# Kernel tuning notes

Hardware: AMD Instinct MI355X
Metric: run time of the kernel (lower is better)

## Reference

```python
import jax, jax.numpy as jnp
import numpy as np

B, S, D, H, E, K = 4, 512, 512, 2048, 8, 2
LN_EPS = 1e-5

def _ln(x, g, b):
    m = jnp.mean(x, axis=-1, keepdims=True)
    v = jnp.var(x, axis=-1, keepdims=True)
    return (x - m) / jnp.sqrt(v + LN_EPS) * g + b

def setup_inputs() -> dict:
    key = jax.random.key(0)
    ks = jax.random.split(key, 8)
    s = 0.02
    return {
        "x": jax.random.normal(ks[0], (B, S, D), dtype=jnp.float32),
        "context": jax.random.normal(ks[1], (B, S, D), dtype=jnp.float32),
        "quality": jax.random.uniform(ks[2], (B, 1), dtype=jnp.float32),
        "rn_g": jnp.ones((D,), jnp.float32), "rn_b": jnp.zeros((D,), jnp.float32),
        "cn_g": jnp.ones((D,), jnp.float32), "cn_b": jnp.zeros((D,), jnp.float32),
        "ctx_W": jax.random.normal(ks[3], (D, D), dtype=jnp.float32) * s,
        "ctx_b": jnp.zeros((D,), jnp.float32),
        "qual_W": jax.random.normal(ks[4], (1, D), dtype=jnp.float32) * s,
        "qual_b": jnp.zeros((D,), jnp.float32),
        "rtr_W": jax.random.normal(ks[5], (D, E), dtype=jnp.float32) * s,
        "rtr_b": jnp.zeros((E,), jnp.float32),
        "temperature": jnp.asarray(1.0, jnp.float32),
        "W1": jax.random.normal(ks[6], (E, D, H), dtype=jnp.float32) * s,
        "b1": jnp.zeros((E, H), jnp.float32),
        "W2": jax.random.normal(ks[7], (E, H, D), dtype=jnp.float32) * s,
        "b2": jnp.zeros((E, D), jnp.float32),
    }

def reference(x, context, quality, rn_g, rn_b, cn_g, cn_b, ctx_W, ctx_b,
              qual_W, qual_b, rtr_W, rtr_b, temperature, W1, b1, W2, b2):
    # router features: LN(x) + context_proj(LN(context)) + quality_proj(quality)
    rf = _ln(x, rn_g, rn_b) + (_ln(context, cn_g, cn_b) @ ctx_W + ctx_b)
    q = quality[:, None, :]                      # [B,1,1]
    rf = rf + (q @ qual_W + qual_b)              # broadcast [B,1,D] over seq
    logits = (rf @ rtr_W + rtr_b) / jnp.maximum(temperature, 0.25)  # [B,S,E]
    # eval mode: no router noise, no dropout
    topk_logits, topk_idx = jax.lax.top_k(logits, K)
    gates = jax.nn.softmax(topk_logits, axis=-1)                    # [B,S,K]
    # per-token per-expert combine weight (equivalent to masked dispatch)
    combine = jnp.sum(gates[..., None] * jax.nn.one_hot(topk_idx, E, dtype=x.dtype), axis=-2)  # [B,S,E]
    # dense all-expert FFN, combined with (mostly zero) gate weights
    h = jax.nn.gelu(jnp.einsum('bsd,edh->bseh', x, W1) + b1, approximate=False)  # [B,S,E,H]
    y = jnp.einsum('bseh,ehd->bsed', h, W2) + b2                                 # [B,S,E,D]
    out = jnp.einsum('bsed,bse->bsd', y, combine)
    # aux losses
    probs = jax.nn.softmax(logits, axis=-1)
    importance = probs.mean(axis=(0, 1))
    load_balance = jnp.mean((importance - 1.0 / E) ** 2)
    router_z = jnp.mean(jax.scipy.special.logsumexp(logits, axis=-1) ** 2)
    entropy = jnp.mean(-jnp.sum(probs * jnp.log(jnp.clip(probs, 1e-9, None)), axis=-1))
    aux = load_balance + 1e-3 * router_z - 1e-3 * entropy
    return out, load_balance, router_z, entropy, aux
```

## Files before the change

kernel.cpp:

```cpp
#include <hip/hip_runtime.h>
#include <hip/hip_bf16.h>
#include <math.h>

#define Bb 4
#define Ss 512
#define Dd 512
#define Hh 2048
#define Ee 8
#define TOKENS 2048
#define CAP 2048

typedef __attribute__((ext_vector_type(8))) _Float16 f16x8;
typedef __attribute__((ext_vector_type(4))) _Float16 f16x4;
typedef __attribute__((ext_vector_type(4))) float f32x4;

#define WS_CNT   0
#define WS_OFFS  32
#define WS_M1    128
#define WS_QV    16512
#define WS_CB    16544
#define WS_LIST  16640
#define WS_GLIST 82176
#define WS_LOG   147712
#define WS_XF    (WS_LOG + 65536)
#define WS_W1F   (WS_XF + 2097152)
#define WS_W2F   (WS_W1F + 16777216)
#define WS_HF    (WS_W2F + 16777216)
#define WS_YB    (WS_HF + 16777216)
#define WS_SEL   (WS_YB + 16777216)

__device__ __forceinline__ float wred(float v) {
#pragma unroll
  for (int o = 32; o > 0; o >>= 1) v += __shfl_down(v, o);
  return v;
}

__device__ __forceinline__ float wredx(float v) {
#pragma unroll
  for (int o = 32; o > 0; o >>= 1) v += __shfl_xor(v, o);
  return v;
}

__device__ __forceinline__ float block_sum(float v, float* s4, int tid) {
  v = wred(v);
  __syncthreads();
  if ((tid & 63) == 0) s4[tid >> 6] = v;
  __syncthreads();
  return s4[0] + s4[1] + s4[2] + s4[3];
}

__device__ __forceinline__ float gelu_f(float v) {
  return 0.5f * v * (1.0f + erff(v * 0.7071067811865475f));
}

#define GL16(gp, lp) __builtin_amdgcn_global_load_lds( \
    (const __attribute__((address_space(1))) void*)(gp), \
    (__attribute__((address_space(3))) void*)(lp), 16, 0, 0)

__device__ __forceinline__ void convT_tile(const float* __restrict__ src,
    _Float16* __restrict__ dst, int R, int C, int bx, float* ls) {
  int nr = R >> 6, ncc = C >> 6;
  int e = bx / (nr * ncc);
  int rem = bx % (nr * ncc);
  int rt = rem / ncc, ct = rem % ncc;
  int tid = threadIdx.x;
  const float* s0 = src + (size_t)e * R * C + (size_t)(rt * 64) * C + ct * 64;
#pragma unroll
  for (int j = 0; j < 4; j++) {
    int li = j * 256 + tid;
    int rr = li >> 4, c4 = (li & 15) << 2;
    float4 v = *(const float4*)(s0 + (size_t)rr * C + c4);
    ls[rr * 65 + c4] = v.x;
    ls[rr * 65 + c4 + 1] = v.y;
    ls[rr * 65 + c4 + 2] = v.z;
    ls[rr * 65 + c4 + 3] = v.w;
  }
  __syncthreads();
#pragma unroll
  for (int j = 0; j < 4; j++) {
    int li = j * 256 + tid;
    int on = li >> 4, k4 = (li & 15) << 2;
    f16x4 o;
    o[0] = (_Float16)ls[(k4 + 0) * 65 + on];
    o[1] = (_Float16)ls[(k4 + 1) * 65 + on];
    o[2] = (_Float16)ls[(k4 + 2) * 65 + on];
    o[3] = (_Float16)ls[(k4 + 3) * 65 + on];
    *(f16x4*)(dst + ((size_t)e * C + ct * 64 + on) * R + rt * 64 + k4) = o;
  }
}

__global__ __launch_bounds__(256) void k_pre(
    const float* __restrict__ ctx_W, const float* __restrict__ rtr_W,
    const float* __restrict__ rtr_b, const float* __restrict__ qual_W,
    const float* __restrict__ qual_b, const float* __restrict__ ctx_b,
    const float* __restrict__ W1, const float* __restrict__ W2,
    float* __restrict__ M1, float* __restrict__ qv, float* __restrict__ cb,
    _Float16* __restrict__ w1f, _Float16* __restrict__ w2f) {
  __shared__ float ls[64 * 65];
  int bx = blockIdx.x;
  if (bx >= 513) {
    int cx = bx - 513;
    if (cx < Ee * 8 * 32) convT_tile(W1, w1f, Dd, Hh, cx, ls);
    else convT_tile(W2, w2f, Hh, Dd, cx - Ee * 8 * 32, ls);
    return;
  }
  int d = bx;
  int tid = threadIdx.x;
  if (tid >= 64) return;
  int lane = tid;
  if (d < Dd) {
    float acc[Ee] = {0.f, 0.f, 0.f, 0.f, 0.f, 0.f, 0.f, 0.f};
    for (int k = lane; k < Dd; k += 64) {
      float cw = ctx_W[d * Dd + k];
      const float* r = rtr_W + k * Ee;
#pragma unroll
      for (int e = 0; e < Ee; e++) acc[e] += cw * r[e];
    }
#pragma unroll
    for (int e = 0; e < Ee; e++) acc[e] = wred(acc[e]);
    if (lane == 0) {
#pragma unroll
      for (int e = 0; e < Ee; e++) M1[d * Ee + e] = acc[e];
    }
  } else {
    float aq[Ee] = {0.f, 0.f, 0.f, 0.f, 0.f, 0.f, 0.f, 0.f};
    float ab[Ee] = {0.f, 0.f, 0.f, 0.f, 0.f, 0.f, 0.f, 0.f};
    for (int k = lane; k < Dd; k += 64) {
      float qw = qual_W[k];
      float bb = ctx_b[k] + qual_b[k];
      const float* r = rtr_W + k * Ee;
#pragma unroll
      for (int e = 0; e < Ee; e++) {
        aq[e] += qw * r[e];
        ab[e] += bb * r[e];
      }
    }
#pragma unroll
    for (int e = 0; e < Ee; e++) {
      aq[e] = wred(aq[e]);
      ab[e] = wred(ab[e]);
    }
    if (lane == 0) {
#pragma unroll
      for (int e = 0; e < Ee; e++) {
        qv[e] = aq[e];
        cb[e] = ab[e] + rtr_b[e];
      }
    }
  }
}

__global__ __launch_bounds__(256) void k_logits(
    const float* __restrict__ x, const float* __restrict__ ctx,
    const float* __restrict__ quality, const float* __restrict__ rn_g,
    const float* __restrict__ rn_b, const float* __restrict__ cn_g,
    const float* __restrict__ cn_b, const float* __restrict__ rtr_W,
    const float* __restrict__ M1, const float* __restrict__ qv,
    const float* __restrict__ cb, const float* __restrict__ temperature,
    float* __restrict__ logitsS, _Float16* __restrict__ xf) {
  int wid = threadIdx.x >> 6, lane = threadIdx.x & 63;
  int t = blockIdx.x * 4 + wid;
  int d0 = lane * 8;

  float xv[8], cv[8];
  *(float4*)&xv[0] = *(const float4*)(x + (size_t)t * Dd + d0);
  *(float4*)&xv[4] = *(const float4*)(x + (size_t)t * Dd + d0 + 4);
  *(float4*)&cv[0] = *(const float4*)(ctx + (size_t)t * Dd + d0);
  *(float4*)&cv[4] = *(const float4*)(ctx + (size_t)t * Dd + d0 + 4);

  f16x8 xh;
#pragma unroll
  for (int d = 0; d < 8; d++) xh[d] = (_Float16)xv[d];
  *(f16x8*)(xf + (size_t)t * Dd + d0) = xh;

  float sx = 0.f, sc = 0.f;
#pragma unroll
  for (int d = 0; d < 8; d++) { sx += xv[d]; sc += cv[d]; }
  float mx = wredx(sx) * (1.f / Dd);
  float mc = wredx(sc) * (1.f / Dd);
  float vx = 0.f, vc = 0.f;
#pragma unroll
  for (int d = 0; d < 8; d++) {
    vx += (xv[d] - mx) * (xv[d] - mx);
    vc += (cv[d] - mc) * (cv[d] - mc);
  }
  float rsx = rsqrtf(wredx(vx) * (1.f / Dd) + 1e-5f);
  float rsc = rsqrtf(wredx(vc) * (1.f / Dd) + 1e-5f);

  float rg[8], rb[8], cg[8], cbb[8];
  *(float4*)&rg[0] = *(const float4*)(rn_g + d0);
  *(float4*)&rg[4] = *(const float4*)(rn_g + d0 + 4);
  *(float4*)&rb[0] = *(const float4*)(rn_b + d0);
  *(float4*)&rb[4] = *(const float4*)(rn_b + d0 + 4);
  *(float4*)&cg[0] = *(const float4*)(cn_g + d0);
  *(float4*)&cg[4] = *(const float4*)(cn_g + d0 + 4);
  *(float4*)&cbb[0] = *(const float4*)(cn_b + d0);
  *(float4*)&cbb[4] = *(const float4*)(cn_b + d0 + 4);

  float lg[Ee] = {0.f, 0.f, 0.f, 0.f, 0.f, 0.f, 0.f, 0.f};
#pragma unroll
  for (int d = 0; d < 8; d++) {
    float xn = (xv[d] - mx) * rsx * rg[d] + rb[d];
    float cn = (cv[d] - mc) * rsc * cg[d] + cbb[d];
    float rw[8], m1[8];
    *(float4*)&rw[0] = *(const float4*)(rtr_W + (size_t)(d0 + d) * Ee);
    *(float4*)&rw[4] = *(const float4*)(rtr_W + (size_t)(d0 + d) * Ee + 4);
    *(float4*)&m1[0] = *(const float4*)(M1 + (size_t)(d0 + d) * Ee);
    *(float4*)&m1[4] = *(const float4*)(M1 + (size_t)(d0 + d) * Ee + 4);
#pragma unroll
    for (int e = 0; e < Ee; e++) lg[e] += xn * rw[e] + cn * m1[e];
  }
#pragma unroll
  for (int e = 0; e < Ee; e++) lg[e] = wredx(lg[e]);

  if (lane == 0) {
    float invT = 1.f / fmaxf(temperature[0], 0.25f);
    float q = quality[t / Ss];
    float L[8];
#pragma unroll
    for (int e = 0; e < Ee; e++) L[e] = (lg[e] + q * qv[e] + cb[e]) * invT;
    *(float4*)(logitsS + (size_t)t * Ee) = *(float4*)&L[0];
    *(float4*)(logitsS + (size_t)t * Ee + 4) = *(float4*)&L[4];
  }
}

__global__ __launch_bounds__(256) void k_select(
    const float* __restrict__ logitsS, int* __restrict__ cnt,
    int* __restrict__ offs, int* __restrict__ list,
    float* __restrict__ glist, int* __restrict__ sel,
    float* __restrict__ out) {
  __shared__ int scnt[Ee];
  __shared__ float s4[4];
  int tid = threadIdx.x;
  if (tid < Ee) scnt[tid] = 0;
  __syncthreads();

  float impL[Ee] = {0.f, 0.f, 0.f, 0.f, 0.f, 0.f, 0.f, 0.f};
  float zL = 0.f, eL = 0.f;

#pragma unroll
  for (int j = 0; j < 8; j++) {
    int t = j * 256 + tid;
    float L[8];
    *(float4*)&L[0] = *(const float4*)(logitsS + (size_t)t * Ee);
    *(float4*)&L[4] = *(const float4*)(logitsS + (size_t)t * Ee + 4);

    int i0 = 0;
#pragma unroll
    for (int e = 1; e < Ee; e++)
      if (L[e] > L[i0]) i0 = e;
    int i1 = (i0 == 0) ? 1 : 0;
#pragma unroll
    for (int e = 0; e < Ee; e++)
      if (e != i0 && L[e] > L[i1]) i1 = e;

    float e1 = __expf(L[i1] - L[i0]);
    float g0 = 1.f / (1.f + e1);
    float g1 = e1 / (1.f + e1);

    float m = L[i0];
    float p[8];
    float sum = 0.f;
#pragma unroll
    for (int e = 0; e < Ee; e++) {
      p[e] = __expf(L[e] - m);
      sum += p[e];
    }
    float lse = m + __logf(sum);
    float inv = 1.f / sum;
    zL += lse * lse;
#pragma unroll
    for (int e = 0; e < Ee; e++) {
      p[e] *= inv;
      eL -= p[e] * __logf(fmaxf(p[e], 1e-9f));
      impL[e] += p[e];
    }

    int s0 = atomicAdd(&scnt[i0], 1);
    list[i0 * CAP + s0] = t;
    glist[i0 * CAP + s0] = g0;
    sel[t * 2 + 0] = (i0 << 12) | s0;
    int s1 = atomicAdd(&scnt[i1], 1);
    list[i1 * CAP + s1] = t;
    glist[i1 * CAP + s1] = g1;
    sel[t * 2 + 1] = (i1 << 12) | s1;
  }

  float impS[Ee];
#pragma unroll
  for (int e = 0; e < Ee; e++) impS[e] = block_sum(impL[e], s4, tid);
  float zS = block_sum(zL, s4, tid);
  float eS = block_sum(eL, s4, tid);
  __syncthreads();

  if (tid == 0) {
    int s = 0;
#pragma unroll
    for (int e = 0; e < Ee; e++) {
      cnt[e] = scnt[e];
      offs[e] = s;
      s += scnt[e];
    }
    float lb = 0.f;
#pragma unroll
    for (int e = 0; e < Ee; e++) {
      float v = impS[e] * (1.f / TOKENS) - (1.f / Ee);
      lb += v * v;
    }
    lb *= (1.f / Ee);
    float rz = zS * (1.f / TOKENS);
    float en = eS * (1.f / TOKENS);
    float* sp = out + (size_t)Bb * Ss * Dd;
    sp[0] = lb;
    sp[1] = rz;
    sp[2] = en;
    sp[3] = lb + 0.001f * rz - 0.001f * en;
  }
}

__global__ __launch_bounds__(256) void k_mg1(
    const _Float16* __restrict__ xf, const _Float16* __restrict__ w1f,
    const float* __restrict__ b1,
    const int* __restrict__ cnt, const int* __restrict__ offs,
    const int* __restrict__ list, _Float16* __restrict__ hf) {
  int bx = blockIdx.x;
  int e = bx >> 8;
  int r = (bx >> 4) & 15;
  int c = bx & 15;
  int ne = cnt[e];
  if (r * 128 >= ne) return;
  int off = offs[e];

  __shared__ _Float16 As[8 * 128 * 8];
  __shared__ _Float16 Bs[8 * 128 * 8];
  __shared__ int stok[128];

  int tid = threadIdx.x;
  if (tid < 128) {
    int row = r * 128 + tid;
    stok[tid] = list[e * CAP + ((row < ne) ? row : (ne - 1))];
  }
  __syncthreads();

  size_t asrc[4], bsrc[4];
  int lq[4];
#pragma unroll
  for (int q = 0; q < 4; q++) {
    int idx = q * 256 + tid;
    int g = idx >> 7, row = idx & 127;
    asrc[q] = (size_t)stok[row] * Dd + g * 8;
    bsrc[q] = ((size_t)(e * Hh + c * 128 + row)) * Dd + g * 8;
    lq[q] = idx * 8;
  }

  int lane = tid & 63, wid = tid >> 6;
  int wm = wid >> 1, wn = wid & 1;
  int l15 = lane & 15, lg = lane >> 4;

  f32x4 acc[4][4] = {};

  for (int k0 = 0; k0 < Dd; k0 += 64) {
#pragma unroll
    for (int q = 0; q < 4; q++) {
      GL16(xf + asrc[q] + k0, &As[lq[q]]);
      GL16(w1f + bsrc[q] + k0, &Bs[lq[q]]);
    }
    __syncthreads();
    f16x8 a[2][4], b[2][4];
#pragma unroll
    for (int ks = 0; ks < 2; ks++) {
#pragma unroll
      for (int m = 0; m < 4; m++)
        a[ks][m] = *(const f16x8*)&As[(((ks * 4 + lg) << 7) + wm * 64 + m * 16 + l15) * 8];
#pragma unroll
      for (int n = 0; n < 4; n++)
        b[ks][n] = *(const f16x8*)&Bs[(((ks * 4 + lg) << 7) + wn * 64 + n * 16 + l15) * 8];
    }
#pragma unroll
    for (int ks = 0; ks < 2; ks++)
#pragma unroll
      for (int m = 0; m < 4; m++)
#pragma unroll
        for (int n = 0; n < 4; n++)
          acc[m][n] = __builtin_amdgcn_mfma_f32_16x16x32_f16(a[ks][m], b[ks][n], acc[m][n], 0, 0, 0);
    __syncthreads();
  }

  int lg4 = lg * 4;
#pragma unroll
  for (int n = 0; n < 4; n++) {
    int colg = c * 128 + wn * 64 + n * 16 + l15;
    float bias = b1[e * Hh + colg];
#pragma unroll
    for (int m = 0; m < 4; m++) {
#pragma unroll
      for (int j = 0; j < 4; j++) {
        int rowl = r * 128 + wm * 64 + m * 16 + lg4 + j;
        if (rowl < ne)
          hf[(size_t)(off + rowl) * Hh + colg] = (_Float16)gelu_f(acc[m][n][j] + bias);
      }
    }
  }
}

__global__ __launch_bounds__(256) void k_mg2(
    const _Float16* __restrict__ hf, const _Float16* __restrict__ w2f,
    const int* __restrict__ cnt, const int* __restrict__ offs,
    _Float16* __restrict__ yb) {
  int bx = blockIdx.x;
  int e = bx >> 8;
  int r = (bx >> 4) & 15;
  int c = (bx >> 2) & 3;
  int kS = bx & 3;
  int ne = cnt[e];
  if (r * 128 >= ne) return;
  int off = offs[e];

  __shared__ _Float16 As[8 * 128 * 8];
  __shared__ _Float16 Bs[8 * 128 * 8];

  int tid = threadIdx.x;
  size_t kbase = (size_t)kS * 512;

  size_t asrc[4], bsrc[4];
  int lq[4];
#pragma unroll
  for (int q = 0; q < 4; q++) {
    int idx = q * 256 + tid;
    int g = idx >> 7, row = idx & 127;
    int ar = r * 128 + row;
    if (ar >= ne) ar = ne - 1;
    asrc[q] = (size_t)(off + ar) * Hh + kbase + g * 8;
    bsrc[q] = ((size_t)(e * Dd + c * 128 + row)) * Hh + kbase + g * 8;
    lq[q] = idx * 8;
  }

  int lane = tid & 63, wid = tid >> 6;
  int wm = wid >> 1, wn = wid & 1;
  int l15 = lane & 15, lg = lane >> 4;

  f32x4 acc[4][4] = {};

  for (int k0 = 0; k0 < 512; k0 += 64) {
#pragma unroll
    for (int q = 0; q < 4; q++) {
      GL16(hf + asrc[q] + k0, &As[lq[q]]);
      GL16(w2f + bsrc[q] + k0, &Bs[lq[q]]);
    }
    __syncthreads();
    f16x8 a[2][4], b[2][4];
#pragma unroll
    for (int ks = 0; ks < 2; ks++) {
#pragma unroll
      for (int m = 0; m < 4; m++)
        a[ks][m] = *(const f16x8*)&As[(((ks * 4 + lg) << 7) + wm * 64 + m * 16 + l15) * 8];
#pragma unroll
      for (int n = 0; n < 4; n++)
        b[ks][n] = *(const f16x8*)&Bs[(((ks * 4 + lg) << 7) + wn * 64 + n * 16 + l15) * 8];
    }
#pragma unroll
    for (int ks = 0; ks < 2; ks++)
#pragma unroll
      for (int m = 0; m < 4; m++)
#pragma unroll
        for (int n = 0; n < 4; n++)
          acc[m][n] = __builtin_amdgcn_mfma_f32_16x16x32_f16(a[ks][m], b[ks][n], acc[m][n], 0, 0, 0);
    __syncthreads();
  }

  int lg4 = lg * 4;
#pragma unroll
  for (int m = 0; m < 4; m++) {
#pragma unroll
    for (int j = 0; j < 4; j++) {
      int rowl = r * 128 + wm * 64 + m * 16 + lg4 + j;
      if (rowl < ne) {
        _Float16* yp = yb + ((size_t)kS * 4096 + off + rowl) * Dd;
#pragma unroll
        for (int n = 0; n < 4; n++) {
          int colg = c * 128 + wn * 64 + n * 16 + l15;
          yp[colg] = (_Float16)acc[m][n][j];
        }
      }
    }
  }
}

__global__ __launch_bounds__(256) void k_comb(
    const _Float16* __restrict__ yb, const int* __restrict__ sel,
    const float* __restrict__ glist, const int* __restrict__ offs,
    const float* __restrict__ b2, float* __restrict__ out) {
  int t = blockIdx.x * 4 + (threadIdx.x >> 6);
  int lane = threadIdx.x & 63;
  int c0 = lane * 8;

  float acc[8] = {0.f, 0.f, 0.f, 0.f, 0.f, 0.f, 0.f, 0.f};
#pragma unroll
  for (int k = 0; k < 2; k++) {
    int pk = sel[t * 2 + k];
    int e = pk >> 12, pos = pk & 4095;
    int slot = offs[e] + pos;
    float g = glist[e * CAP + pos];
    float pa[8] = {0.f, 0.f, 0.f, 0.f, 0.f, 0.f, 0.f, 0.f};
#pragma unroll
    for (int s = 0; s < 4; s++) {
      f16x8 v = *(const f16x8*)(yb + ((size_t)s * 4096 + slot) * Dd + c0);
#pragma unroll
      for (int j = 0; j < 8; j++) pa[j] += (float)v[j];
    }
    const float* bb = b2 + e * Dd + c0;
    float b4[8];
    *(float4*)&b4[0] = *(const float4*)bb;
    *(float4*)&b4[4] = *(const float4*)(bb + 4);
#pragma unroll
    for (int j = 0; j < 8; j++) acc[j] += g * (pa[j] + b4[j]);
  }
  float* op = out + (size_t)t * Dd + c0;
  *(float4*)op = *(float4*)&acc[0];
  *(float4*)(op + 4) = *(float4*)&acc[4];
}

extern "C" void kernel_launch(void* const* d_in, const int* in_sizes, int n_in,
                              void* d_out, int out_size, void* d_ws, size_t ws_size,
                              hipStream_t stream) {
  const float* x = (const float*)d_in[0];
  const float* ctx = (const float*)d_in[1];
  const float* quality = (const float*)d_in[2];
  const float* rn_g = (const float*)d_in[3];
  const float* rn_b = (const float*)d_in[4];
  const float* cn_g = (const float*)d_in[5];
  const float* cn_b = (const float*)d_in[6];
  const float* ctx_W = (const float*)d_in[7];
  const float* ctx_b = (const float*)d_in[8];
  const float* qual_W = (const float*)d_in[9];
  const float* qual_b = (const float*)d_in[10];
  const float* rtr_W = (const float*)d_in[11];
  const float* rtr_b = (const float*)d_in[12];
  const float* temperature = (const float*)d_in[13];
  const float* W1 = (const float*)d_in[14];
  const float* b1 = (const float*)d_in[15];
  const float* W2 = (const float*)d_in[16];
  const float* b2 = (const float*)d_in[17];
  float* out = (float*)d_out;

  char* w = (char*)d_ws;
  int* cnt = (int*)(w + WS_CNT);
  int* offs = (int*)(w + WS_OFFS);
  float* M1 = (float*)(w + WS_M1);
  float* qv = (float*)(w + WS_QV);
  float* cb = (float*)(w + WS_CB);
  int* list = (int*)(w + WS_LIST);
  float* glist = (float*)(w + WS_GLIST);
  float* logitsS = (float*)(w + WS_LOG);
  _Float16* xf = (_Float16*)(w + WS_XF);
  _Float16* w1f = (_Float16*)(w + WS_W1F);
  _Float16* w2f = (_Float16*)(w + WS_W2F);
  _Float16* hf = (_Float16*)(w + WS_HF);
  _Float16* yb = (_Float16*)(w + WS_YB);
  int* sel = (int*)(w + WS_SEL);

  k_pre<<<513 + Ee * 8 * 32 * 2, 256, 0, stream>>>(
      ctx_W, rtr_W, rtr_b, qual_W, qual_b, ctx_b, W1, W2, M1, qv, cb, w1f, w2f);
  k_logits<<<TOKENS / 4, 256, 0, stream>>>(x, ctx, quality, rn_g, rn_b, cn_g, cn_b, rtr_W,
                                           M1, qv, cb, temperature, logitsS, xf);
  k_select<<<1, 256, 0, stream>>>(logitsS, cnt, offs, list, glist, sel, out);
  k_mg1<<<Ee * 16 * 16, 256, 0, stream>>>(xf, w1f, b1, cnt, offs, list, hf);
  k_mg2<<<Ee * 16 * 4 * 4, 256, 0, stream>>>(hf, w2f, cnt, offs, yb);
  k_comb<<<TOKENS / 4, 256, 0, stream>>>(yb, sel, glist, offs, b2, out);
}
```

Before: 256.7 us.

## Pad expert segments to tiles, pre-gather tokens, and move routing math into logits kernel

The top-k selection, gates and aux-loss statistics are now computed per token in the logits kernel, with per-block partial sums, so the single-block select kernel only does the scatter and a small reduction. Each expert segment is padded to a multiple of 128 rows, and a new gather kernel copies the routed token rows contiguously. The GEMM kernels therefore use a compact grid over padded tiles with contiguous A loads and no row bounds checks. In exchange there is an extra gather pass plus wasted work on padding rows, but far fewer empty blocks are launched and the serial single-block work shrinks.

```diff
diff --git a/kernel.cpp b/kernel.cpp
--- a/kernel.cpp
+++ b/kernel.cpp
@@ -9,25 +9,29 @@
 #define Ee 8
 #define TOKENS 2048
 #define CAP 2048
+#define SLOTS 5120
 
 typedef __attribute__((ext_vector_type(8))) _Float16 f16x8;
 typedef __attribute__((ext_vector_type(4))) _Float16 f16x4;
 typedef __attribute__((ext_vector_type(4))) float f32x4;
 
 #define WS_CNT   0
-#define WS_OFFS  32
-#define WS_M1    128
-#define WS_QV    16512
-#define WS_CB    16544
-#define WS_LIST  16640
-#define WS_GLIST 82176
-#define WS_LOG   147712
-#define WS_XF    (WS_LOG + 65536)
-#define WS_W1F   (WS_XF + 2097152)
-#define WS_W2F   (WS_W1F + 16777216)
-#define WS_HF    (WS_W2F + 16777216)
-#define WS_YB    (WS_HF + 16777216)
-#define WS_SEL   (WS_YB + 16777216)
+#define WS_OFFSP 32
+#define WS_TK    128
+#define WS_GT    8320
+#define WS_STAT  24704
+#define WS_M1    45184
+#define WS_QV    61568
+#define WS_CB    61600
+#define WS_LIST  61664
+#define WS_GLIST 127200
+#define WS_SEL   192736
+#define WS_XF    262144
+#define WS_W1F   2359296
+#define WS_W2F   19136512
+#define WS_XG    35913728
+#define WS_HF    41156608
+#define WS_YB    62128128
 
 __device__ __forceinline__ float wred(float v) {
 #pragma unroll
@@ -157,7 +161,9 @@
     const float* __restrict__ cn_b, const float* __restrict__ rtr_W,
     const float* __restrict__ M1, const float* __restrict__ qv,
     const float* __restrict__ cb, const float* __restrict__ temperature,
-    float* __restrict__ logitsS, _Float16* __restrict__ xf) {
+    _Float16* __restrict__ xf, int* __restrict__ tk,
+    float2* __restrict__ gates, float* __restrict__ stats) {
+  __shared__ float sst[4][10];
   int wid = threadIdx.x >> 6, lane = threadIdx.x & 63;
   int t = blockIdx.x * 4 + wid;
   int d0 = lane * 8;
@@ -219,14 +225,53 @@
     float L[8];
 #pragma unroll
     for (int e = 0; e < Ee; e++) L[e] = (lg[e] + q * qv[e] + cb[e]) * invT;
-    *(float4*)(logitsS + (size_t)t * Ee) = *(float4*)&L[0];
-    *(float4*)(logitsS + (size_t)t * Ee + 4) = *(float4*)&L[4];
-  }
+
+    int i0 = 0;
+#pragma unroll
+    for (int e = 1; e < Ee; e++)
+      if (L[e] > L[i0]) i0 = e;
+    int i1 = (i0 == 0) ? 1 : 0;
+#pragma unroll
+    for (int e = 0; e < Ee; e++)
+      if (e != i0 && L[e] > L[i1]) i1 = e;
+
+    float e1 = __expf(L[i1] - L[i0]);
+    float g0 = 1.f / (1.f + e1);
+    float g1 = e1 / (1.f + e1);
+    tk[t] = (i0 << 3) | i1;
+    gates[t] = make_float2(g0, g1);
+
+    float m = L[i0];
+    float p[8];
+    float sum = 0.f;
+#pragma unroll
+    for (int e = 0; e < Ee; e++) {
+      p[e] = __expf(L[e] - m);
+      sum += p[e];
+    }
+    float lse = m + __logf(sum);
+    float inv = 1.f / sum;
+    float ent = 0.f;
+#pragma unroll
+    for (int e = 0; e < Ee; e++) {
+      p[e] *= inv;
+      ent -= p[e] * __logf(fmaxf(p[e], 1e-9f));
+      sst[wid][e] = p[e];
+    }
+    sst[wid][8] = lse * lse;
+    sst[wid][9] = ent;
+  }
+  __syncthreads();
+  int tid = threadIdx.x;
+  if (tid < 10)
+    stats[blockIdx.x * 10 + tid] =
+        sst[0][tid] + sst[1][tid] + sst[2][tid] + sst[3][tid];
 }
 
 __global__ __launch_bounds__(256) void k_select(
-    const float* __restrict__ logitsS, int* __restrict__ cnt,
-    int* __restrict__ offs, int* __restrict__ list,
+    const int* __restrict__ tk, const float2* __restrict__ gates,
+    const float* __restrict__ stats, int* __restrict__ cnt,
+    int* __restrict__ offsP, int* __restrict__ list,
     float* __restrict__ glist, int* __restrict__ sel,
     float* __restrict__ out) {
   __shared__ int scnt[Ee];
@@ -235,81 +280,50 @@
   if (tid < Ee) scnt[tid] = 0;
   __syncthreads();
 
-  float impL[Ee] = {0.f, 0.f, 0.f, 0.f, 0.f, 0.f, 0.f, 0.f};
-  float zL = 0.f, eL = 0.f;
-
 #pragma unroll
   for (int j = 0; j < 8; j++) {
     int t = j * 256 + tid;
-    float L[8];
-    *(float4*)&L[0] = *(const float4*)(logitsS + (size_t)t * Ee);
-    *(float4*)&L[4] = *(const float4*)(logitsS + (size_t)t * Ee + 4);
-
-    int i0 = 0;
-#pragma unroll
-    for (int e = 1; e < Ee; e++)
-      if (L[e] > L[i0]) i0 = e;
-    int i1 = (i0 == 0) ? 1 : 0;
-#pragma unroll
-    for (int e = 0; e < Ee; e++)
-      if (e != i0 && L[e] > L[i1]) i1 = e;
-
-    float e1 = __expf(L[i1] - L[i0]);
-    float g0 = 1.f / (1.f + e1);
-    float g1 = e1 / (1.f + e1);
-
-    float m = L[i0];
-    float p[8];
-    float sum = 0.f;
-#pragma unroll
-    for (int e = 0; e < Ee; e++) {
-      p[e] = __expf(L[e] - m);
-      sum += p[e];
-    }
-    float lse = m + __logf(sum);
-    float inv = 1.f / sum;
-    zL += lse * lse;
-#pragma unroll
-    for (int e = 0; e < Ee; e++) {
-      p[e] *= inv;
-      eL -= p[e] * __logf(fmaxf(p[e], 1e-9f));
-      impL[e] += p[e];
-    }
-
+    int pk = tk[t];
+    int i0 = (pk >> 3) & 7, i1 = pk & 7;
+    float2 g = gates[t];
     int s0 = atomicAdd(&scnt[i0], 1);
     list[i0 * CAP + s0] = t;
-    glist[i0 * CAP + s0] = g0;
+    glist[i0 * CAP + s0] = g.x;
     sel[t * 2 + 0] = (i0 << 12) | s0;
     int s1 = atomicAdd(&scnt[i1], 1);
     list[i1 * CAP + s1] = t;
-    glist[i1 * CAP + s1] = g1;
+    glist[i1 * CAP + s1] = g.y;
     sel[t * 2 + 1] = (i1 << 12) | s1;
   }
-
-  float impS[Ee];
-#pragma unroll
-  for (int e = 0; e < Ee; e++) impS[e] = block_sum(impL[e], s4, tid);
-  float zS = block_sum(zL, s4, tid);
-  float eS = block_sum(eL, s4, tid);
   __syncthreads();
+
+  float rc[10];
+#pragma unroll
+  for (int c = 0; c < 10; c++)
+    rc[c] = stats[tid * 10 + c] + stats[(tid + 256) * 10 + c];
+  float rs[10];
+#pragma unroll
+  for (int c = 0; c < 10; c++) rs[c] = block_sum(rc[c], s4, tid);
 
   if (tid == 0) {
     int s = 0;
 #pragma unroll
     for (int e = 0; e < Ee; e++) {
       cnt[e] = scnt[e];
-      offs[e] = s;
-      s += scnt[e];
-    }
+      offsP[e] = s;
+      s += ((scnt[e] + 127) >> 7) << 7;
+    }
+    offsP[Ee] = s;
+
     float lb = 0.f;
 #pragma unroll
     for (int e = 0; e < Ee; e++) {
-      float v = impS[e] * (1.f / TOKENS) - (1.f / Ee);
+      float v = rs[e] * (1.f / TOKENS) - (1.f / Ee);
       lb += v * v;
     }
     lb *= (1.f / Ee);
-    float rz = zS * (1.f / TOKENS);
-    float en = eS * (1.f / TOKENS);
+    float rz = rs[8] * (1.f / TOKENS);
+    float en = rs[9] * (1.f / TOKENS);
     float* sp = out + (size_t)Bb * Ss * Dd;
     sp[0] = lb;
     sp[1] = rz;
@@ -318,37 +332,50 @@
   }
 }
 
+__global__ __launch_bounds__(256) void k_gather(
+    const _Float16* __restrict__ xf, const int* __restrict__ cnt,
+    const int* __restrict__ offsP, const int* __restrict__ list,
+    _Float16* __restrict__ xg) {
+  int s = blockIdx.x * 4 + (threadIdx.x >> 6);
+  int lane = threadIdx.x & 63;
+  int e = 0;
+#pragma unroll
+  for (int q = 0; q < 7; q++)
+    if (s >= offsP[q + 1]) e = q + 1;
+  int pos = s - offsP[e];
+  f16x8 v = {};
+  if (s < offsP[Ee] && pos < cnt[e]) {
+    int t = list[e * CAP + pos];
+    v = *(const f16x8*)(xf + (size_t)t * Dd + lane * 8);
+  }
+  *(f16x8*)(xg + (size_t)s * Dd + lane * 8) = v;
+}
+
 __global__ __launch_bounds__(256) void k_mg1(
-    const _Float16* __restrict__ xf, const _Float16* __restrict__ w1f,
-    const float* __restrict__ b1,
-    const int* __restrict__ cnt, const int* __restrict__ offs,
-    const int* __restrict__ list, _Float16* __restrict__ hf) {
+    const _Float16* __restrict__ xg, const _Float16* __restrict__ w1f,
+    const float* __restrict__ b1, const int* __restrict__ offsP,
+    _Float16* __restrict__ hf) {
   int bx = blockIdx.x;
-  int e = bx >> 8;
-  int r = (bx >> 4) & 15;
+  int r = bx >> 4;
   int c = bx & 15;
-  int ne = cnt[e];
-  if (r * 128 >= ne) return;
-  int off = offs[e];
+  int totalP = offsP[Ee];
+  if (r * 128 >= totalP) return;
+  int e = 0;
+#pragma unroll
+  for (int q = 0; q < 7; q++)
+    if (r * 128 >= offsP[q + 1]) e = q + 1;
 
   __shared__ _Float16 As[8 * 128 * 8];
   __shared__ _Float16 Bs[8 * 128 * 8];
-  __shared__ int stok[128];
 
   int tid = threadIdx.x;
-  if (tid < 128) {
-    int row = r * 128 + tid;
-    stok[tid] = list[e * CAP + ((row < ne) ? row : (ne - 1))];
-  }
-  __syncthreads();
-
   size_t asrc[4], bsrc[4];
   int lq[4];
 #pragma unroll
   for (int q = 0; q < 4; q++) {
     int idx = q * 256 + tid;
     int g = idx >> 7, row = idx & 127;
-    asrc[q] = (size_t)stok[row] * Dd + g * 8;
+    asrc[q] = (size_t)(r * 128 + row) * Dd + g * 8;
     bsrc[q] = ((size_t)(e * Hh + c * 128 + row)) * Dd + g * 8;
     lq[q] = idx * 8;
   }
@@ -362,7 +389,7 @@
   for (int k0 = 0; k0 < Dd; k0 += 64) {
 #pragma unroll
     for (int q = 0; q < 4; q++) {
-      GL16(xf + asrc[q] + k0, &As[lq[q]]);
+      GL16(xg + asrc[q] + k0, &As[lq[q]]);
       GL16(w1f + bsrc[q] + k0, &Bs[lq[q]]);
     }
     __syncthreads();
@@ -396,8 +423,7 @@
 #pragma unroll
       for (int j = 0; j < 4; j++) {
         int rowl = r * 128 + wm * 64 + m * 16 + lg4 + j;
-        if (rowl < ne)
-          hf[(size_t)(off + rowl) * Hh + colg] = (_Float16)gelu_f(acc[m][n][j] + bias);
+        hf[(size_t)rowl * Hh + colg] = (_Float16)gelu_f(acc[m][n][j] + bias);
       }
     }
   }
@@ -405,16 +431,17 @@
 
 __global__ __launch_bounds__(256) void k_mg2(
     const _Float16* __restrict__ hf, const _Float16* __restrict__ w2f,
-    const int* __restrict__ cnt, const int* __restrict__ offs,
-    _Float16* __restrict__ yb) {
+    const int* __restrict__ offsP, _Float16* __restrict__ yb) {
   int bx = blockIdx.x;
-  int e = bx >> 8;
-  int r = (bx >> 4) & 15;
+  int r = bx >> 4;
   int c = (bx >> 2) & 3;
   int kS = bx & 3;
-  int ne = cnt[e];
-  if (r * 128 >= ne) return;
-  int off = offs[e];
+  int totalP = offsP[Ee];
+  if (r * 128 >= totalP) return;
+  int e = 0;
+#pragma unroll
+  for (int q = 0; q < 7; q++)
+    if (r * 128 >= offsP[q + 1]) e = q + 1;
 
   __shared__ _Float16 As[8 * 128 * 8];
   __shared__ _Float16 Bs[8 * 128 * 8];
@@ -428,9 +455,7 @@
   for (int q = 0; q < 4; q++) {
     int idx = q * 256 + tid;
     int g = idx >> 7, row = idx & 127;
-    int ar = r * 128 + row;
-    if (ar >= ne) ar = ne - 1;
-    asrc[q] = (size_t)(off + ar) * Hh + kbase + g * 8;
+    asrc[q] = (size_t)(r * 128 + row) * Hh + kbase + g * 8;
     bsrc[q] = ((size_t)(e * Dd + c * 128 + row)) * Hh + kbase + g * 8;
     lq[q] = idx * 8;
   }
@@ -474,13 +499,11 @@
 #pragma unroll
     for (int j = 0; j < 4; j++) {
       int rowl = r * 128 + wm * 64 + m * 16 + lg4 + j;
-      if (rowl < ne) {
-        _Float16* yp = yb + ((size_t)kS * 4096 + off + rowl) * Dd;
-#pragma unroll
-        for (int n = 0; n < 4; n++) {
-          int colg = c * 128 + wn * 64 + n * 16 + l15;
-          yp[colg] = (_Float16)acc[m][n][j];
-        }
+      _Float16* yp = yb + ((size_t)kS * SLOTS + rowl) * Dd;
+#pragma unroll
+      for (int n = 0; n < 4; n++) {
+        int colg = c * 128 + wn * 64 + n * 16 + l15;
+        yp[colg] = (_Float16)acc[m][n][j];
       }
     }
   }
@@ -488,7 +511,7 @@
 
 __global__ __launch_bounds__(256) void k_comb(
     const _Float16* __restrict__ yb, const int* __restrict__ sel,
-    const float* __restrict__ glist, const int* __restrict__ offs,
+    const float* __restrict__ glist, const int* __restrict__ offsP,
     const float* __restrict__ b2, float* __restrict__ out) {
   int t = blockIdx.x * 4 + (threadIdx.x >> 6);
   int lane = threadIdx.x & 63;
@@ -499,12 +522,12 @@
   for (int k = 0; k < 2; k++) {
     int pk = sel[t * 2 + k];
     int e = pk >> 12, pos = pk & 4095;
-    int slot = offs[e] + pos;
+    int slot = offsP[e] + pos;
     float g = glist[e * CAP + pos];
     float pa[8] = {0.f, 0.f, 0.f, 0.f, 0.f, 0.f, 0.f, 0.f};
 #pragma unroll
     for (int s = 0; s < 4; s++) {
-      f16x8 v = *(const f16x8*)(yb + ((size_t)s * 4096 + slot) * Dd + c0);
+      f16x8 v = *(const f16x8*)(yb + ((size_t)s * SLOTS + slot) * Dd + c0);
 #pragma unroll
       for (int j = 0; j < 8; j++) pa[j] += (float)v[j];
     }
@@ -545,26 +568,30 @@
 
   char* w = (char*)d_ws;
   int* cnt = (int*)(w + WS_CNT);
-  int* offs = (int*)(w + WS_OFFS);
+  int* offsP = (int*)(w + WS_OFFSP);
+  int* tk = (int*)(w + WS_TK);
+  float2* gates = (float2*)(w + WS_GT);
+  float* stats = (float*)(w + WS_STAT);
   float* M1 = (float*)(w + WS_M1);
   float* qv = (float*)(w + WS_QV);
   float* cb = (float*)(w + WS_CB);
   int* list = (int*)(w + WS_LIST);
   float* glist = (float*)(w + WS_GLIST);
-  float* logitsS = (float*)(w + WS_LOG);
+  int* sel = (int*)(w + WS_SEL);
   _Float16* xf = (_Float16*)(w + WS_XF);
   _Float16* w1f = (_Float16*)(w + WS_W1F);
   _Float16* w2f = (_Float16*)(w + WS_W2F);
+  _Float16* xg = (_Float16*)(w + WS_XG);
   _Float16* hf = (_Float16*)(w + WS_HF);
   _Float16* yb = (_Float16*)(w + WS_YB);
-  int* sel = (int*)(w + WS_SEL);
 
   k_pre<<<513 + Ee * 8 * 32 * 2, 256, 0, stream>>>(
       ctx_W, rtr_W, rtr_b, qual_W, qual_b, ctx_b, W1, W2, M1, qv, cb, w1f, w2f);
   k_logits<<<TOKENS / 4, 256, 0, stream>>>(x, ctx, quality, rn_g, rn_b, cn_g, cn_b, rtr_W,
-                                           M1, qv, cb, temperature, logitsS, xf);
-  k_select<<<1, 256, 0, stream>>>(logitsS, cnt, offs, list, glist, sel, out);
-  k_mg1<<<Ee * 16 * 16, 256, 0, stream>>>(xf, w1f, b1, cnt, offs, list, hf);
-  k_mg2<<<Ee * 16 * 4 * 4, 256, 0, stream>>>(hf, w2f, cnt, offs, yb);
-  k_comb<<<TOKENS / 4, 256, 0, stream>>>(yb, sel, glist, offs, b2, out);
-}
+                                           M1, qv, cb, temperature, xf, tk, gates, stats);
+  k_select<<<1, 256, 0, stream>>>(tk, gates, stats, cnt, offsP, list, glist, sel, out);
+  k_gather<<<SLOTS / 4, 256, 0, stream>>>(xf, cnt, offsP, list, xg);
+  k_mg1<<<40 * 16, 256, 0, stream>>>(xg, w1f, b1, offsP, hf);
+  k_mg2<<<40 * 4 * 4, 256, 0, stream>>>(hf, w2f, offsP, yb);
+  k_comb<<<TOKENS / 4, 256, 0, stream>>>(yb, sel, glist, offsP, b2, out);
+}
```

After: 238.5 us. 7.1% less time.
